# Optimization experiments

Hardware: AMD Instinct MI355X
Metric: run time of the kernel (lower is better)

Reference implementation:

```python
import jax, jax.numpy as jnp
import numpy as np

# dims: B graphs, E entities, R relations, N = E + R nodes, H hidden, P prop steps
B, N, E, R, H, P, RT, NH = 4, 2048, 1600, 448, 512, 2, 100, 4
DH = H // NH  # head dim = 128


def setup_inputs() -> dict:
    key = jax.random.key(0)
    ks = jax.random.split(key, 12)
    adj = jax.random.randint(ks[0], (B, N, N), 0, 2, dtype=jnp.int32)
    # self-loops so no attention row is fully masked (avoids NaN softmax rows)
    adj = jnp.maximum(adj, jnp.eye(N, dtype=jnp.int32)[None])
    rels = jax.random.randint(ks[1], (B, R), 0, RT, dtype=jnp.int32)
    vents = jax.random.normal(ks[2], (B, E, H), jnp.float32)
    renc_w = jax.random.normal(ks[3], (RT, H), jnp.float32) * 0.05  # xavier-ish
    s = 0.02
    inp = dict(adjs=adj, rels=rels, vents=vents, entlen=E, renc_w=renc_w)
    inp["Wq"] = jax.random.normal(ks[4], (P, H, H), jnp.float32) * s
    inp["Wk"] = jax.random.normal(ks[5], (P, H, H), jnp.float32) * s
    inp["Wv"] = jax.random.normal(ks[6], (P, H, H), jnp.float32) * s
    inp["Wo"] = jax.random.normal(ks[7], (P, H, H), jnp.float32) * s
    inp["W1"] = jax.random.normal(ks[8], (P, H, 4 * H), jnp.float32) * s
    inp["W2"] = jax.random.normal(ks[9], (P, 4 * H, H), jnp.float32) * s
    inp["bq"] = jnp.zeros((P, H), jnp.float32)
    inp["bk"] = jnp.zeros((P, H), jnp.float32)
    inp["bv"] = jnp.zeros((P, H), jnp.float32)
    inp["bo"] = jnp.zeros((P, H), jnp.float32)
    inp["b1"] = jnp.zeros((P, 4 * H), jnp.float32)
    inp["b2"] = jnp.zeros((P, H), jnp.float32)
    inp["ln1_g"] = jnp.ones((P, H), jnp.float32)
    inp["ln1_b"] = jnp.zeros((P, H), jnp.float32)
    inp["ln2_g"] = jnp.ones((P, H), jnp.float32)
    inp["ln2_b"] = jnp.zeros((P, H), jnp.float32)
    inp["prelu_a"] = jnp.full((P, 4 * H), 0.25, jnp.float32)  # torch PReLU default
    return inp


def _ln(x, g, b):
    mu = x.mean(-1, keepdims=True)
    var = x.var(-1, keepdims=True)
    return (x - mu) * jax.lax.rsqrt(var + jnp.float32(1e-5)) * g + b


def reference(adjs, rels, vents, entlen, renc_w, Wq, Wk, Wv, Wo, W1, W2,
              bq, bk, bv, bo, b1, b2, ln1_g, ln1_b, ln2_g, ln2_b, prelu_a):
    vrel = renc_w[rels]                              # (B,R,H) relation embeddings
    x = jnp.concatenate([vents, vrel], axis=1)       # (B,N,H) graph node features
    neg = (adjs == 0)[:, None, :, :]                 # (B,1,N,N) True = masked
    for j in range(P):  # prop steps, structurally distinct layers
        q = (x @ Wq[j] + bq[j]).reshape(B, N, NH, DH)
        k = (x @ Wk[j] + bk[j]).reshape(B, N, NH, DH)
        v = (x @ Wv[j] + bv[j]).reshape(B, N, NH, DH)
        sc = jnp.einsum('bqhd,bkhd->bhqk', q, k) / jnp.sqrt(jnp.float32(DH))
        sc = jnp.where(neg, jnp.float32(-1e9), sc)
        a = jax.nn.softmax(sc, axis=-1)
        o = jnp.einsum('bhqk,bkhd->bqhd', a, v).reshape(B, N, H)
        attn_out = o @ Wo[j] + bo[j]
        t = _ln(attn_out, ln1_g[j], ln1_b[j])        # ln_1
        hpre = t @ W1[j] + b1[j]
        hact = jnp.where(hpre >= 0, hpre, prelu_a[j] * hpre)  # PReLU
        y = hact @ W2[j] + b2[j]                     # dropout is identity in eval
        x = _ln(y + t, ln2_g[j], ln2_b[j])           # ln_2 residual
    glob = x[:, entlen]                              # (B,H) global node = vgraph[entlens[i]]
    gents = x                                        # (B,N,H) all graphs same size -> no pad
    elens = jnp.full((B,), N, jnp.int32)
    emask = jnp.arange(N)[None, :] <= elens[:, None] # (B,N) faithful `<=` comparison
    return glob, gents, emask
```

## Files before the change

kernel.cpp:

```cpp
#include <hip/hip_runtime.h>

typedef unsigned short u16;
typedef __bf16 bf16x8 __attribute__((ext_vector_type(8)));
typedef float floatx4 __attribute__((ext_vector_type(4)));


__device__ __forceinline__ float bf2f(u16 u) {
  union { unsigned int i; float f; } c; c.i = ((unsigned int)u) << 16; return c.f;
}
__device__ __forceinline__ u16 f2bf(float f) {
  union { unsigned int i; float f; } c; c.f = f;
  unsigned int i = c.i;
  return (u16)((i + 0x7FFFu + ((i >> 16) & 1u)) >> 16);
}

template <int EPI, int FOUT>
__global__ __launch_bounds__(256, 2) void gemm_tn(
    const u16* __restrict__ A, const u16* __restrict__ Bt, void* __restrict__ Cv,
    const float* __restrict__ bias, const float* __restrict__ alpha,
    const float* __restrict__ res, int K, int lda, int ldb, int ldc) {
  __shared__ __align__(16) u16 As[128 * 32];
  __shared__ __align__(16) u16 Bs[128 * 32];

  const int tid = threadIdx.x;
  const int w = tid >> 6, lane = tid & 63;
  const int quad = lane >> 4, l16 = lane & 15;
  const int wm = w & 1, wn = w >> 1;

  const int slot0 = w * 128 + lane;
  const int slot1 = slot0 + 64;
  const u16* pA0 = A + (long)(blockIdx.x * 128 + (slot0 >> 2)) * lda + (slot0 & 3) * 8;
  const u16* pA1 = A + (long)(blockIdx.x * 128 + (slot1 >> 2)) * lda + (slot1 & 3) * 8;
  const u16* pB0 = Bt + (long)(blockIdx.y * 128 + (slot0 >> 2)) * ldb + (slot0 & 3) * 8;
  const u16* pB1 = Bt + (long)(blockIdx.y * 128 + (slot1 >> 2)) * ldb + (slot1 & 3) * 8;

  const floatx4 z4 = {0.f, 0.f, 0.f, 0.f};
  floatx4 acc[4][4];
#pragma unroll
  for (int i = 0; i < 4; i++)
#pragma unroll
    for (int j = 0; j < 4; j++) acc[i][j] = z4;

  for (int k0 = 0; k0 < K; k0 += 32) {
    int4 a0 = *(const int4*)pA0;
    int4 a1 = *(const int4*)pA1;
    int4 b0 = *(const int4*)pB0;
    int4 b1 = *(const int4*)pB1;
    pA0 += 32; pA1 += 32; pB0 += 32; pB1 += 32;
    __syncthreads();
    *(int4*)&As[slot0 * 8] = a0;
    *(int4*)&As[slot1 * 8] = a1;
    *(int4*)&Bs[slot0 * 8] = b0;
    *(int4*)&Bs[slot1 * 8] = b1;
    __syncthreads();

    bf16x8 af[4], bv[4];
#pragma unroll
    for (int mi = 0; mi < 4; mi++)
      af[mi] = *(const bf16x8*)&As[(wm * 64 + mi * 16 + l16) * 32 + quad * 8];
#pragma unroll
    for (int ni = 0; ni < 4; ni++)
      bv[ni] = *(const bf16x8*)&Bs[(wn * 64 + ni * 16 + l16) * 32 + quad * 8];
#pragma unroll
    for (int mi = 0; mi < 4; mi++)
#pragma unroll
      for (int ni = 0; ni < 4; ni++)
        acc[mi][ni] = __builtin_amdgcn_mfma_f32_16x16x32_bf16(af[mi], bv[ni], acc[mi][ni], 0, 0, 0);
  }

  const long crow0 = (long)blockIdx.x * 128;
  const int ncol0 = blockIdx.y * 128 + wn * 64 + l16;
#pragma unroll
  for (int mi = 0; mi < 4; mi++) {
#pragma unroll
    for (int r = 0; r < 4; r++) {
      const int m = wm * 64 + mi * 16 + quad * 4 + r;
      const long rowbase = (crow0 + m) * (long)ldc;
      const float* rrow = (EPI == 3) ? (res + rowbase) : nullptr;
#pragma unroll
      for (int ni = 0; ni < 4; ni++) {
        const int n = ncol0 + ni * 16;
        float vv = acc[mi][ni][r] + bias[n];
        if (EPI == 2) { if (vv < 0.f) vv *= alpha[n]; }
        if (EPI == 3) vv += rrow[n];
        if (FOUT) ((float*)Cv)[rowbase + n] = vv;
        else ((u16*)Cv)[rowbase + n] = f2bf(vv);
      }
    }
  }
}

#define LDP 136
__global__ __launch_bounds__(256, 3) void k_attn(
    const u16* __restrict__ qg, const u16* __restrict__ kg,
    const u16* __restrict__ vt, const unsigned* __restrict__ mbits,
    u16* __restrict__ og) {
  __shared__ __align__(16) u16 KV[128 * LDP];
  __shared__ __align__(16) u16 Pl[64 * LDP];
  __shared__ unsigned Ml[64 * 4];

  const int tid = threadIdx.x;
  const int w = tid >> 6, lane = tid & 63;
  const int quad = lane >> 4, l16 = lane & 15;
  const int qt = blockIdx.x;
  const int z = blockIdx.y;
  const int b = z >> 2, h = z & 3;

  const u16* qbase = qg + (long)b * 2048 * 512 + h * 128;
  const u16* kbase = kg + (long)b * 2048 * 512 + h * 128;
  const u16* vbase = vt + (long)(b * 4 + h) * 128 * 2048;
  const unsigned* mbase = mbits + ((long)b * 2048 + qt * 64) * 64;

  bf16x8 qf[4];
#pragma unroll
  for (int ks = 0; ks < 4; ks++)
    qf[ks] = *(const bf16x8*)(qbase +
        (long)(qt * 64 + w * 16 + l16) * 512 + ks * 32 + quad * 8);

  const floatx4 z4 = {0.f, 0.f, 0.f, 0.f};
  floatx4 Oacc[8];
#pragma unroll
  for (int ni = 0; ni < 8; ni++) Oacc[ni] = z4;
  float mrow[4], lrow[4];
#pragma unroll
  for (int r = 0; r < 4; r++) { mrow[r] = -3.4e38f; lrow[r] = 0.f; }

  const float scale = 0.08838834764831845f;
  const int srow = tid >> 4;
  const int scol = (tid & 15) * 8;

  for (int kt = 0; kt < 16; kt++) {
    __syncthreads();
#pragma unroll
    for (int rr = 0; rr < 128; rr += 16)
      *(int4*)&KV[(rr + srow) * LDP + scol] =
          *(const int4*)(kbase + (long)(kt * 128 + rr + srow) * 512 + scol);
    Ml[tid] = mbase[(tid >> 2) * 64 + kt * 4 + (tid & 3)];
    __syncthreads();

    floatx4 accS[8];
#pragma unroll
    for (int ni = 0; ni < 8; ni++) accS[ni] = z4;
#pragma unroll
    for (int ks = 0; ks < 4; ks++) {
      bf16x8 bf[8];
#pragma unroll
      for (int ni = 0; ni < 8; ni++)
        bf[ni] = *(const bf16x8*)&KV[(ni * 16 + l16) * LDP + ks * 32 + quad * 8];
#pragma unroll
      for (int ni = 0; ni < 8; ni++)
        accS[ni] = __builtin_amdgcn_mfma_f32_16x16x32_bf16(qf[ks], bf[ni], accS[ni], 0, 0, 0);
    }
    __syncthreads();

#pragma unroll
    for (int rr = 0; rr < 128; rr += 16)
      *(int4*)&KV[(rr + srow) * LDP + scol] =
          *(const int4*)(vbase + (long)(rr + srow) * 2048 + kt * 128 + scol);

#pragma unroll
    for (int r = 0; r < 4; r++) {
      const int rowl = w * 16 + quad * 4 + r;
      float s[8];
      float rmax = -1e30f;
#pragma unroll
      for (int ni = 0; ni < 8; ni++) {
        const unsigned mw = Ml[rowl * 4 + (ni >> 1)];
        const int on = (mw >> ((ni & 1) * 16 + l16)) & 1;
        s[ni] = on ? accS[ni][r] * scale : -1e30f;
        rmax = fmaxf(rmax, s[ni]);
      }
#pragma unroll
      for (int off = 1; off < 16; off <<= 1) rmax = fmaxf(rmax, __shfl_xor(rmax, off, 64));
      const float mnew = fmaxf(mrow[r], rmax);
      const float al = __expf(mrow[r] - mnew);
      float rs = 0.f;
#pragma unroll
      for (int ni = 0; ni < 8; ni++) {
        const float pp = __expf(s[ni] - mnew);
        rs += pp;
        Pl[rowl * LDP + ni * 16 + l16] = f2bf(pp);
      }
#pragma unroll
      for (int off = 1; off < 16; off <<= 1) rs += __shfl_xor(rs, off, 64);
      lrow[r] = lrow[r] * al + rs;
      mrow[r] = mnew;
#pragma unroll
      for (int ni = 0; ni < 8; ni++) Oacc[ni][r] *= al;
    }
    __syncthreads();

#pragma unroll
    for (int ks = 0; ks < 4; ks++) {
      bf16x8 bv[8];
#pragma unroll
      for (int ni = 0; ni < 8; ni++)
        bv[ni] = *(const bf16x8*)&KV[(ni * 16 + l16) * LDP + ks * 32 + quad * 8];
      bf16x8 pf = *(const bf16x8*)&Pl[(w * 16 + l16) * LDP + ks * 32 + quad * 8];
#pragma unroll
      for (int ni = 0; ni < 8; ni++)
        Oacc[ni] = __builtin_amdgcn_mfma_f32_16x16x32_bf16(pf, bv[ni], Oacc[ni], 0, 0, 0);
    }
  }

#pragma unroll
  for (int r = 0; r < 4; r++) {
    const float inv = 1.f / lrow[r];
    const long q = qt * 64 + w * 16 + quad * 4 + r;
#pragma unroll
    for (int ni = 0; ni < 8; ni++)
      og[((long)b * 2048 + q) * 512 + h * 128 + ni * 16 + l16] = f2bf(Oacc[ni][r] * inv);
  }
}

__global__ __launch_bounds__(256) void k_maskpack(const int* __restrict__ adjs,
                                                  unsigned* __restrict__ bits) {
  const int wid = blockIdx.x * 4 + (threadIdx.x >> 6);
  const int lane = threadIdx.x & 63;
  const unsigned long long bal = __ballot(adjs[(long)wid * 64 + lane] != 0);
  if (lane == 0) {
    bits[wid * 2] = (unsigned)bal;
    bits[wid * 2 + 1] = (unsigned)(bal >> 32);
  }
}

__global__ __launch_bounds__(256) void tr_w(const float* __restrict__ src, u16* __restrict__ dst,
                                            int ld_src, int ld_dst, long s_z, long d_z) {
  __shared__ u16 tile[32][33];
  src += (long)blockIdx.z * s_z;
  dst += (long)blockIdx.z * d_z;
  const int r0 = blockIdx.x << 5, c0 = blockIdx.y << 5;
  const int tx = threadIdx.x & 31, ty = threadIdx.x >> 5;
#pragma unroll
  for (int i = 0; i < 32; i += 8)
    tile[ty + i][tx] = f2bf(src[(long)(r0 + ty + i) * ld_src + c0 + tx]);
  __syncthreads();
#pragma unroll
  for (int i = 0; i < 32; i += 8)
    dst[(long)(c0 + ty + i) * ld_dst + r0 + tx] = tile[tx][ty + i];
}

__global__ __launch_bounds__(256) void tr_bf16(const u16* __restrict__ src, u16* __restrict__ dst,
                                               int ld_src, int ld_dst, int zdiv,
                                               long s_out, long s_in, long d_out, long d_in_) {
  __shared__ u16 tile[32][33];
  const int zz = blockIdx.z, zq = zz / zdiv, zr = zz % zdiv;
  src += (long)zq * s_out + (long)zr * s_in;
  dst += (long)zq * d_out + (long)zr * d_in_;
  const int r0 = blockIdx.x << 5, c0 = blockIdx.y << 5;
  const int tx = threadIdx.x & 31, ty = threadIdx.x >> 5;
#pragma unroll
  for (int i = 0; i < 32; i += 8) tile[ty + i][tx] = src[(long)(r0 + ty + i) * ld_src + c0 + tx];
  __syncthreads();
#pragma unroll
  for (int i = 0; i < 32; i += 8) dst[(long)(c0 + ty + i) * ld_dst + r0 + tx] = tile[tx][ty + i];
}

__global__ __launch_bounds__(256) void k_build_x(const float* __restrict__ vents,
                                                 const int* __restrict__ rels,
                                                 const float* __restrict__ renc,
                                                 float* __restrict__ x, u16* __restrict__ xb) {
  const long idx = (long)blockIdx.x * 256 + threadIdx.x;
  const int c = (int)(idx & 511);
  const int row = (int)(idx >> 9);
  const int b = row >> 11, n = row & 2047;
  float val;
  if (n < 1600) val = vents[((long)b * 1600 + n) * 512 + c];
  else val = renc[(long)rels[b * 448 + (n - 1600)] * 512 + c];
  x[idx] = val;
  xb[idx] = f2bf(val);
}

__global__ __launch_bounds__(256) void k_ln(const float* __restrict__ in, float* __restrict__ out,
                                            u16* __restrict__ outb,
                                            const float* __restrict__ g, const float* __restrict__ bb) {
  __shared__ float rs[256], rq[256];
  const int row = blockIdx.x, tid = threadIdx.x;
  const float* p = in + (long)row * 512;
  const float a0 = p[tid], a1 = p[tid + 256];
  rs[tid] = a0 + a1;
  rq[tid] = a0 * a0 + a1 * a1;
  __syncthreads();
  for (int s = 128; s > 0; s >>= 1) {
    if (tid < s) { rs[tid] += rs[tid + s]; rq[tid] += rq[tid + s]; }
    __syncthreads();
  }
  const float mu = rs[0] * (1.f / 512.f);
  const float var = rq[0] * (1.f / 512.f) - mu * mu;
  const float inv = 1.0f / sqrtf(var + 1e-5f);
  const float o0 = (a0 - mu) * inv * g[tid] + bb[tid];
  const float o1 = (a1 - mu) * inv * g[tid + 256] + bb[tid + 256];
  out[(long)row * 512 + tid] = o0;
  out[(long)row * 512 + tid + 256] = o1;
  outb[(long)row * 512 + tid] = f2bf(o0);
  outb[(long)row * 512 + tid + 256] = f2bf(o1);
}

__global__ __launch_bounds__(256) void k_out(const float* __restrict__ x, const int* __restrict__ entlen,
                                             float* __restrict__ out, long out_n) {
  const long idx = (long)blockIdx.x * 256 + threadIdx.x;
  if (idx >= out_n) return;
  const long G = 2048, GE = 2048 + 4194304;
  float v;
  if (idx < G) {
    const int b = (int)(idx >> 9), c = (int)(idx & 511);
    int e = entlen[0];
    if (e < 0 || e >= 2048) e = 1600;
    v = x[((long)b * 2048 + e) * 512 + c];
  } else if (idx < GE) {
    v = x[idx - G];
  } else {
    v = 1.0f;
  }
  out[idx] = v;
}

extern "C" void kernel_launch(void* const* d_in, const int* in_sizes, int n_in,
                              void* d_out, int out_size, void* d_ws, size_t ws_size,
                              hipStream_t stream) {
  const int* adjs = (const int*)d_in[0];
  const int* rels = (const int*)d_in[1];
  const float* vents = (const float*)d_in[2];
  const int* entlen = (const int*)d_in[3];
  const float* renc = (const float*)d_in[4];
  const float* Wq = (const float*)d_in[5];
  const float* Wk = (const float*)d_in[6];
  const float* Wv = (const float*)d_in[7];
  const float* Wo = (const float*)d_in[8];
  const float* W1 = (const float*)d_in[9];
  const float* W2 = (const float*)d_in[10];
  const float* bq = (const float*)d_in[11];
  const float* bk = (const float*)d_in[12];
  const float* bv = (const float*)d_in[13];
  const float* bo = (const float*)d_in[14];
  const float* b1 = (const float*)d_in[15];
  const float* b2 = (const float*)d_in[16];
  const float* ln1g = (const float*)d_in[17];
  const float* ln1b = (const float*)d_in[18];
  const float* ln2g = (const float*)d_in[19];
  const float* ln2b = (const float*)d_in[20];
  const float* prelu = (const float*)d_in[21];

  char* base = (char*)d_ws;
  float* x_f   = (float*)(base + 0);
  float* t_f   = (float*)(base + 16777216);
  float* tmp_f = (float*)(base + 33554432);
  u16* wt  = (u16*)(base + 50331648);
  u16* xb  = (u16*)(base + 62914560);
  u16* tb  = (u16*)(base + 71303168);
  u16* qb  = (u16*)(base + 79691776);
  u16* kb  = (u16*)(base + 88080384);
  u16* vb  = (u16*)(base + 96468992);
  u16* Vtb = (u16*)(base + 104857600);
  u16* ob  = (u16*)(base + 113246208);
  u16* hb  = (u16*)(base + 121634816);
  unsigned* mbits = (unsigned*)(base + 155189248);

  k_build_x<<<dim3(16384), 256, 0, stream>>>(vents, rels, renc, x_f, xb);
  k_maskpack<<<dim3(65536), 256, 0, stream>>>(adjs, mbits);

  tr_w<<<dim3(16, 16, 2), 256, 0, stream>>>(Wq, wt + 0,       512, 512, 262144L, 3145728L);
  tr_w<<<dim3(16, 16, 2), 256, 0, stream>>>(Wk, wt + 262144,  512, 512, 262144L, 3145728L);
  tr_w<<<dim3(16, 16, 2), 256, 0, stream>>>(Wv, wt + 524288,  512, 512, 262144L, 3145728L);
  tr_w<<<dim3(16, 16, 2), 256, 0, stream>>>(Wo, wt + 786432,  512, 512, 262144L, 3145728L);
  tr_w<<<dim3(16, 64, 2), 256, 0, stream>>>(W1, wt + 1048576, 2048, 512, 1048576L, 3145728L);
  tr_w<<<dim3(64, 16, 2), 256, 0, stream>>>(W2, wt + 2097152, 512, 2048, 1048576L, 3145728L);

  for (int j = 0; j < 2; j++) {
    const u16* wqt = wt + (long)j * 3145728;
    const u16* wkt = wqt + 262144;
    const u16* wvt = wqt + 524288;
    const u16* wot = wqt + 786432;
    const u16* w1t = wqt + 1048576;
    const u16* w2t = wqt + 2097152;

    gemm_tn<1, 0><<<dim3(64, 4), 256, 0, stream>>>(xb, wqt, qb, bq + j * 512, nullptr, nullptr, 512, 512, 512, 512);
    gemm_tn<1, 0><<<dim3(64, 4), 256, 0, stream>>>(xb, wkt, kb, bk + j * 512, nullptr, nullptr, 512, 512, 512, 512);
    gemm_tn<1, 0><<<dim3(64, 4), 256, 0, stream>>>(xb, wvt, vb, bv + j * 512, nullptr, nullptr, 512, 512, 512, 512);

    tr_bf16<<<dim3(64, 4, 16), 256, 0, stream>>>(vb, Vtb, 512, 2048, 4,
        1048576L, 128L, 1048576L, 262144L);

    k_attn<<<dim3(32, 16), 256, 0, stream>>>(qb, kb, Vtb, mbits, ob);

    gemm_tn<1, 1><<<dim3(64, 4), 256, 0, stream>>>(ob, wot, tmp_f, bo + j * 512, nullptr, nullptr, 512, 512, 512, 512);
    k_ln<<<dim3(8192), 256, 0, stream>>>(tmp_f, t_f, tb, ln1g + j * 512, ln1b + j * 512);
    gemm_tn<2, 0><<<dim3(64, 16), 256, 0, stream>>>(tb, w1t, hb, b1 + j * 2048, prelu + j * 2048, nullptr, 512, 512, 512, 2048);
    gemm_tn<3, 1><<<dim3(64, 4), 256, 0, stream>>>(hb, w2t, tmp_f, b2 + j * 512, nullptr, t_f, 2048, 2048, 2048, 512);
    k_ln<<<dim3(8192), 256, 0, stream>>>(tmp_f, x_f, xb, ln2g + j * 512, ln2b + j * 512);
  }

  const long out_n = (long)out_size;
  k_out<<<dim3((unsigned)((out_n + 255) / 256)), 256, 0, stream>>>(x_f, entlen, (float*)d_out, out_n);
}
```

Baseline: 688.0 us.

## Fuse QKV projections into one GEMM, pad LDS, add 64-wide tile GEMM

The three Q/K/V projection GEMMs become a single launch writing an interleaved 1536-wide QKV buffer, with the bias chosen per column segment. Attention and the V transpose now read from that buffer with stride 1536. The shared-memory tiles are padded to 40 elements per row to cut bank conflicts, and launch bounds are raised to allow 3 blocks per CU. The 512-wide output GEMMs (Wo and W2) switch to a 128x64 tile variant to double the grid and fill more CUs, at the cost of more A-tile reloads.

After: 642.9 us. -6.5%, faster.

```diff
diff --git a/kernel.cpp b/kernel.cpp
--- a/kernel.cpp
+++ b/kernel.cpp
@@ -14,13 +14,16 @@
   return (u16)((i + 0x7FFFu + ((i >> 16) & 1u)) >> 16);
 }
 
-template <int EPI, int FOUT>
-__global__ __launch_bounds__(256, 2) void gemm_tn(
+#define GP 40
+
+template <int EPI, int FOUT, int SEG3>
+__global__ __launch_bounds__(256, 3) void gemm_tn(
     const u16* __restrict__ A, const u16* __restrict__ Bt, void* __restrict__ Cv,
-    const float* __restrict__ bias, const float* __restrict__ alpha,
+    const float* __restrict__ bias, const float* __restrict__ bias2,
+    const float* __restrict__ bias3, const float* __restrict__ alpha,
     const float* __restrict__ res, int K, int lda, int ldb, int ldc) {
-  __shared__ __align__(16) u16 As[128 * 32];
-  __shared__ __align__(16) u16 Bs[128 * 32];
+  __shared__ __align__(16) u16 As[128 * GP];
+  __shared__ __align__(16) u16 Bs[128 * GP];
 
   const int tid = threadIdx.x;
   const int w = tid >> 6, lane = tid & 63;
@@ -29,10 +32,12 @@
 
   const int slot0 = w * 128 + lane;
   const int slot1 = slot0 + 64;
-  const u16* pA0 = A + (long)(blockIdx.x * 128 + (slot0 >> 2)) * lda + (slot0 & 3) * 8;
-  const u16* pA1 = A + (long)(blockIdx.x * 128 + (slot1 >> 2)) * lda + (slot1 & 3) * 8;
-  const u16* pB0 = Bt + (long)(blockIdx.y * 128 + (slot0 >> 2)) * ldb + (slot0 & 3) * 8;
-  const u16* pB1 = Bt + (long)(blockIdx.y * 128 + (slot1 >> 2)) * ldb + (slot1 & 3) * 8;
+  const int r0 = slot0 >> 2, c0 = (slot0 & 3) * 8;
+  const int r1 = slot1 >> 2, c1 = (slot1 & 3) * 8;
+  const u16* pA0 = A + (long)(blockIdx.x * 128 + r0) * lda + c0;
+  const u16* pA1 = A + (long)(blockIdx.x * 128 + r1) * lda + c1;
+  const u16* pB0 = Bt + (long)(blockIdx.y * 128 + r0) * ldb + c0;
+  const u16* pB1 = Bt + (long)(blockIdx.y * 128 + r1) * ldb + c1;
 
   const floatx4 z4 = {0.f, 0.f, 0.f, 0.f};
   floatx4 acc[4][4];
@@ -48,19 +53,19 @@
     int4 b1 = *(const int4*)pB1;
     pA0 += 32; pA1 += 32; pB0 += 32; pB1 += 32;
     __syncthreads();
-    *(int4*)&As[slot0 * 8] = a0;
-    *(int4*)&As[slot1 * 8] = a1;
-    *(int4*)&Bs[slot0 * 8] = b0;
-    *(int4*)&Bs[slot1 * 8] = b1;
+    *(int4*)&As[r0 * GP + c0] = a0;
+    *(int4*)&As[r1 * GP + c1] = a1;
+    *(int4*)&Bs[r0 * GP + c0] = b0;
+    *(int4*)&Bs[r1 * GP + c1] = b1;
     __syncthreads();
 
     bf16x8 af[4], bv[4];
 #pragma unroll
     for (int mi = 0; mi < 4; mi++)
-      af[mi] = *(const bf16x8*)&As[(wm * 64 + mi * 16 + l16) * 32 + quad * 8];
+      af[mi] = *(const bf16x8*)&As[(wm * 64 + mi * 16 + l16) * GP + quad * 8];
 #pragma unroll
     for (int ni = 0; ni < 4; ni++)
-      bv[ni] = *(const bf16x8*)&Bs[(wn * 64 + ni * 16 + l16) * 32 + quad * 8];
+      bv[ni] = *(const bf16x8*)&Bs[(wn * 64 + ni * 16 + l16) * GP + quad * 8];
 #pragma unroll
     for (int mi = 0; mi < 4; mi++)
 #pragma unroll
@@ -68,6 +73,11 @@
         acc[mi][ni] = __builtin_amdgcn_mfma_f32_16x16x32_bf16(af[mi], bv[ni], acc[mi][ni], 0, 0, 0);
   }
 
+  const float* bptr = bias;
+  if (SEG3) {
+    const int seg = blockIdx.y >> 2;
+    bptr = (seg == 0) ? bias : ((seg == 1) ? bias2 : bias3);
+  }
   const long crow0 = (long)blockIdx.x * 128;
   const int ncol0 = blockIdx.y * 128 + wn * 64 + l16;
 #pragma unroll
@@ -75,6 +85,78 @@
 #pragma unroll
     for (int r = 0; r < 4; r++) {
       const int m = wm * 64 + mi * 16 + quad * 4 + r;
+      const long rowbase = (crow0 + m) * (long)ldc;
+      const float* rrow = (EPI == 3) ? (res + rowbase) : nullptr;
+#pragma unroll
+      for (int ni = 0; ni < 4; ni++) {
+        const int n = ncol0 + ni * 16;
+        float vv = acc[mi][ni][r] + bptr[SEG3 ? (n & 511) : n];
+        if (EPI == 2) { if (vv < 0.f) vv *= alpha[n]; }
+        if (EPI == 3) vv += rrow[n];
+        if (FOUT) ((float*)Cv)[rowbase + n] = vv;
+        else ((u16*)Cv)[rowbase + n] = f2bf(vv);
+      }
+    }
+  }
+}
+
+template <int EPI, int FOUT>
+__global__ __launch_bounds__(256, 3) void gemm_tn64(
+    const u16* __restrict__ A, const u16* __restrict__ Bt, void* __restrict__ Cv,
+    const float* __restrict__ bias, const float* __restrict__ alpha,
+    const float* __restrict__ res, int K, int lda, int ldb, int ldc) {
+  __shared__ __align__(16) u16 As[128 * GP];
+  __shared__ __align__(16) u16 Bs[64 * GP];
+
+  const int tid = threadIdx.x;
+  const int w = tid >> 6, lane = tid & 63;
+  const int quad = lane >> 4, l16 = lane & 15;
+
+  const int rA0 = tid >> 2, cA = (tid & 3) * 8;
+  const int rA1 = rA0 + 64;
+  const u16* pA0 = A + (long)(blockIdx.x * 128 + rA0) * lda + cA;
+  const u16* pA1 = A + (long)(blockIdx.x * 128 + rA1) * lda + cA;
+  const u16* pB  = Bt + (long)(blockIdx.y * 64 + rA0) * ldb + cA;
+
+  const floatx4 z4 = {0.f, 0.f, 0.f, 0.f};
+  floatx4 acc[2][4];
+#pragma unroll
+  for (int i = 0; i < 2; i++)
+#pragma unroll
+    for (int j = 0; j < 4; j++) acc[i][j] = z4;
+
+  for (int k0 = 0; k0 < K; k0 += 32) {
+    int4 a0 = *(const int4*)pA0;
+    int4 a1 = *(const int4*)pA1;
+    int4 b0 = *(const int4*)pB;
+    pA0 += 32; pA1 += 32; pB += 32;
+    __syncthreads();
+    *(int4*)&As[rA0 * GP + cA] = a0;
+    *(int4*)&As[rA1 * GP + cA] = a1;
+    *(int4*)&Bs[rA0 * GP + cA] = b0;
+    __syncthreads();
+
+    bf16x8 af[2], bv[4];
+#pragma unroll
+    for (int mi = 0; mi < 2; mi++)
+      af[mi] = *(const bf16x8*)&As[(w * 32 + mi * 16 + l16) * GP + quad * 8];
+#pragma unroll
+    for (int ni = 0; ni < 4; ni++)
+      bv[ni] = *(const bf16x8*)&Bs[(ni * 16 + l16) * GP + quad * 8];
+#pragma unroll
+    for (int mi = 0; mi < 2; mi++)
+#pragma unroll
+      for (int ni = 0; ni < 4; ni++)
+        acc[mi][ni] = __builtin_amdgcn_mfma_f32_16x16x32_bf16(af[mi], bv[ni], acc[mi][ni], 0, 0, 0);
+  }
+
+  const long crow0 = (long)blockIdx.x * 128;
+  const int ncol0 = blockIdx.y * 64 + l16;
+#pragma unroll
+  for (int mi = 0; mi < 2; mi++) {
+#pragma unroll
+    for (int r = 0; r < 4; r++) {
+      const int m = w * 32 + mi * 16 + quad * 4 + r;
       const long rowbase = (crow0 + m) * (long)ldc;
       const float* rrow = (EPI == 3) ? (res + rowbase) : nullptr;
 #pragma unroll
@@ -92,9 +174,8 @@
 
 #define LDP 136
 __global__ __launch_bounds__(256, 3) void k_attn(
-    const u16* __restrict__ qg, const u16* __restrict__ kg,
-    const u16* __restrict__ vt, const unsigned* __restrict__ mbits,
-    u16* __restrict__ og) {
+    const u16* __restrict__ qkv, const u16* __restrict__ vt,
+    const unsigned* __restrict__ mbits, u16* __restrict__ og) {
   __shared__ __align__(16) u16 KV[128 * LDP];
   __shared__ __align__(16) u16 Pl[64 * LDP];
   __shared__ unsigned Ml[64 * 4];
@@ -106,8 +187,8 @@
   const int z = blockIdx.y;
   const int b = z >> 2, h = z & 3;
 
-  const u16* qbase = qg + (long)b * 2048 * 512 + h * 128;
-  const u16* kbase = kg + (long)b * 2048 * 512 + h * 128;
+  const u16* qbase = qkv + (long)b * 2048 * 1536 + h * 128;
+  const u16* kbase = qbase + 512;
   const u16* vbase = vt + (long)(b * 4 + h) * 128 * 2048;
   const unsigned* mbase = mbits + ((long)b * 2048 + qt * 64) * 64;
 
@@ -115,7 +196,7 @@
 #pragma unroll
   for (int ks = 0; ks < 4; ks++)
     qf[ks] = *(const bf16x8*)(qbase +
-        (long)(qt * 64 + w * 16 + l16) * 512 + ks * 32 + quad * 8);
+        (long)(qt * 64 + w * 16 + l16) * 1536 + ks * 32 + quad * 8);
 
   const floatx4 z4 = {0.f, 0.f, 0.f, 0.f};
   floatx4 Oacc[8];
@@ -134,7 +215,7 @@
 #pragma unroll
     for (int rr = 0; rr < 128; rr += 16)
       *(int4*)&KV[(rr + srow) * LDP + scol] =
-          *(const int4*)(kbase + (long)(kt * 128 + rr + srow) * 512 + scol);
+          *(const int4*)(kbase + (long)(kt * 128 + rr + srow) * 1536 + scol);
     Ml[tid] = mbase[(tid >> 2) * 64 + kt * 4 + (tid & 3)];
     __syncthreads();
 
@@ -348,9 +429,7 @@
   u16* wt  = (u16*)(base + 50331648);
   u16* xb  = (u16*)(base + 62914560);
   u16* tb  = (u16*)(base + 71303168);
-  u16* qb  = (u16*)(base + 79691776);
-  u16* kb  = (u16*)(base + 88080384);
-  u16* vb  = (u16*)(base + 96468992);
+  u16* qkv = (u16*)(base + 79691776);
   u16* Vtb = (u16*)(base + 104857600);
   u16* ob  = (u16*)(base + 113246208);
   u16* hb  = (u16*)(base + 121634816);
@@ -368,25 +447,23 @@
 
   for (int j = 0; j < 2; j++) {
     const u16* wqt = wt + (long)j * 3145728;
-    const u16* wkt = wqt + 262144;
-    const u16* wvt = wqt + 524288;
     const u16* wot = wqt + 786432;
     const u16* w1t = wqt + 1048576;
     const u16* w2t = wqt + 2097152;
 
-    gemm_tn<1, 0><<<dim3(64, 4), 256, 0, stream>>>(xb, wqt, qb, bq + j * 512, nullptr, nullptr, 512, 512, 512, 512);
-    gemm_tn<1, 0><<<dim3(64, 4), 256, 0, stream>>>(xb, wkt, kb, bk + j * 512, nullptr, nullptr, 512, 512, 512, 512);
-    gemm_tn<1, 0><<<dim3(64, 4), 256, 0, stream>>>(xb, wvt, vb, bv + j * 512, nullptr, nullptr, 512, 512, 512, 512);
-
-    tr_bf16<<<dim3(64, 4, 16), 256, 0, stream>>>(vb, Vtb, 512, 2048, 4,
-        1048576L, 128L, 1048576L, 262144L);
-
-    k_attn<<<dim3(32, 16), 256, 0, stream>>>(qb, kb, Vtb, mbits, ob);
-
-    gemm_tn<1, 1><<<dim3(64, 4), 256, 0, stream>>>(ob, wot, tmp_f, bo + j * 512, nullptr, nullptr, 512, 512, 512, 512);
+    gemm_tn<1, 0, 1><<<dim3(64, 12), 256, 0, stream>>>(
+        xb, wqt, qkv, bq + j * 512, bk + j * 512, bv + j * 512, nullptr, nullptr,
+        512, 512, 512, 1536);
+
+    tr_bf16<<<dim3(64, 4, 16), 256, 0, stream>>>(qkv + 1024, Vtb, 1536, 2048, 4,
+        3145728L, 128L, 1048576L, 262144L);
+
+    k_attn<<<dim3(32, 16), 256, 0, stream>>>(qkv, Vtb, mbits, ob);
+
+    gemm_tn64<1, 1><<<dim3(64, 8), 256, 0, stream>>>(ob, wot, tmp_f, bo + j * 512, nullptr, nullptr, 512, 512, 512, 512);
     k_ln<<<dim3(8192), 256, 0, stream>>>(tmp_f, t_f, tb, ln1g + j * 512, ln1b + j * 512);
-    gemm_tn<2, 0><<<dim3(64, 16), 256, 0, stream>>>(tb, w1t, hb, b1 + j * 2048, prelu + j * 2048, nullptr, 512, 512, 512, 2048);
-    gemm_tn<3, 1><<<dim3(64, 4), 256, 0, stream>>>(hb, w2t, tmp_f, b2 + j * 512, nullptr, t_f, 2048, 2048, 2048, 512);
+    gemm_tn<2, 0, 0><<<dim3(64, 16), 256, 0, stream>>>(tb, w1t, hb, b1 + j * 2048, nullptr, nullptr, prelu + j * 2048, nullptr, 512, 512, 512, 2048);
+    gemm_tn64<3, 1><<<dim3(64, 8), 256, 0, stream>>>(hb, w2t, tmp_f, b2 + j * 512, nullptr, t_f, 2048, 2048, 2048, 512);
     k_ln<<<dim3(8192), 256, 0, stream>>>(tmp_f, x_f, xb, ln2g + j * 512, ln2b + j * 512);
   }
 
```
